# Optimization experiments

Hardware: AMD Instinct MI355X
Metric: run time of the kernel (lower is better)

## Reference

```python
import jax, jax.numpy as jnp
import numpy as np

WIN = 9
PAD = WIN // 2    # floor(9/2) = 4
WIN_SIZE = WIN * WIN
EPS = 1e-05


def _box_sum(x):
    # 9x9 ones-kernel conv, stride 1, pad 4 (SAME size), NCHW with C=1
    filt = jnp.ones((1, 1, WIN, WIN), dtype=x.dtype)
    return jax.lax.conv_general_dilated(
        x, filt, window_strides=(1, 1),
        padding=[(PAD, PAD), (PAD, PAD)],
        dimension_numbers=('NCHW', 'OIHW', 'NCHW'))


def setup_inputs() -> dict:
    key = jax.random.key(0)
    k1, k2 = jax.random.split(key)
    I = jax.random.normal(k1, (8, 1, 1024, 1024), dtype=jnp.float32)
    J = jax.random.normal(k2, (8, 1, 1024, 1024), dtype=jnp.float32)
    return {"I": I, "J": J}


def reference(I, J):
    I_sum = _box_sum(I)
    J_sum = _box_sum(J)
    I2_sum = _box_sum(I * I)
    J2_sum = _box_sum(J * J)
    IJ_sum = _box_sum(I * J)

    u_I = I_sum / WIN_SIZE
    u_J = J_sum / WIN_SIZE

    cross = IJ_sum - u_J * I_sum - u_I * J_sum + u_I * u_J * WIN_SIZE
    I_var = I2_sum - 2 * u_I * I_sum + u_I * u_I * WIN_SIZE
    J_var = J2_sum - 2 * u_J * J_sum + u_J * u_J * WIN_SIZE

    cc = cross * cross / (I_var * J_var + EPS)
    return jnp.mean(cc)
```

## Files before the change

### kernel.cpp

```cpp
#include <hip/hip_runtime.h>

#define H 1024
#define W 1024
#define NIMG 8
#define TX 128
#define CY 8
#define RS_ROWS (CY + 8)
#define NBX (W / TX)
#define NBY (H / CY)
#define NBLOCKS (NBX * NBY * NIMG)
#define EPS 1e-5f

__global__ __launch_bounds__(256, 4)
void ncc_main(const float* __restrict__ I, const float* __restrict__ J,
              float* __restrict__ partial) {
  __shared__ float4 rs4[RS_ROWS][TX];
  __shared__ float  rs1[RS_ROWS][TX];

  const int tid = threadIdx.x;
  const int gx = blockIdx.x, gy = blockIdx.y, n = blockIdx.z;
  const size_t img_off = (size_t)n * H * W;

  {
    const int r  = tid >> 4;
    const int xg = tid & 15;
    const int y  = gy * CY + r - 4;
    float a[16], b[16];
    if (y >= 0 && y < H) {
      const int xbase = gx * TX + xg * 8 - 4;
      const float* Ip = I + img_off + (size_t)y * W;
      const float* Jp = J + img_off + (size_t)y * W;
      if (xbase >= 0 && xbase + 16 <= W) {
        const float4* pa = reinterpret_cast<const float4*>(Ip + xbase);
        const float4* pb = reinterpret_cast<const float4*>(Jp + xbase);
        #pragma unroll
        for (int q = 0; q < 4; ++q) {
          float4 va = pa[q], vb = pb[q];
          a[4*q+0] = va.x; a[4*q+1] = va.y; a[4*q+2] = va.z; a[4*q+3] = va.w;
          b[4*q+0] = vb.x; b[4*q+1] = vb.y; b[4*q+2] = vb.z; b[4*q+3] = vb.w;
        }
      } else {
        #pragma unroll
        for (int k = 0; k < 16; ++k) {
          int xx = xbase + k;
          bool in = (xx >= 0) && (xx < W);
          a[k] = in ? Ip[xx] : 0.0f;
          b[k] = in ? Jp[xx] : 0.0f;
        }
      }
    } else {
      #pragma unroll
      for (int k = 0; k < 16; ++k) { a[k] = 0.0f; b[k] = 0.0f; }
    }
    float sI = 0.f, sJ = 0.f, sII = 0.f, sJJ = 0.f, sIJ = 0.f;
    #pragma unroll
    for (int k = 0; k < 9; ++k) {
      sI  += a[k];        sJ  += b[k];
      sII += a[k] * a[k]; sJJ += b[k] * b[k];
      sIJ += a[k] * b[k];
    }
    const int xg8 = xg * 8;
    const int xm  = xg & 7;
    #pragma unroll
    for (int i = 0; i < 8; ++i) {
      if (i > 0) {
        float an = a[i+8], al = a[i-1], bn = b[i+8], bl = b[i-1];
        sI  += an - al;           sJ  += bn - bl;
        sII += an*an - al*al;     sJJ += bn*bn - bl*bl;
        sIJ += an*bn - al*bl;
      }
      const int px = xg8 + (i ^ xm);
      rs4[r][px] = make_float4(sI, sJ, sII, sJJ);
      rs1[r][px] = sIJ;
    }
  }
  __syncthreads();

  const int x  = tid & 127;
  const int h  = tid >> 7;
  const int xs = (x & ~7) | ((x ^ (x >> 3)) & 7);
  const int base = h * 4;
  float4 rows4[9]; float rows1[9];
  float wI = 0.f, wJ = 0.f, wII = 0.f, wJJ = 0.f, wIJ = 0.f;
  #pragma unroll
  for (int k = 0; k < 9; ++k) {
    rows4[k] = rs4[base + k][xs];
    rows1[k] = rs1[base + k][xs];
    wI += rows4[k].x; wJ += rows4[k].y; wII += rows4[k].z; wJJ += rows4[k].w;
    wIJ += rows1[k];
  }
  const float inv81 = 1.0f / 81.0f;
  float acc = 0.f;
  #pragma unroll
  for (int i = 0; i < 4; ++i) {
    if (i > 0) {
      float4 e4 = rs4[base + 8 + i][xs];
      float  e1 = rs1[base + 8 + i][xs];
      wI  += e4.x - rows4[i-1].x;  wJ  += e4.y - rows4[i-1].y;
      wII += e4.z - rows4[i-1].z;  wJJ += e4.w - rows4[i-1].w;
      wIJ += e1   - rows1[i-1];
    }
    float cross = wIJ - wI * wJ * inv81;
    float Iv    = wII - wI * wI * inv81;
    float Jv    = wJJ - wJ * wJ * inv81;
    acc += cross * cross / (Iv * Jv + EPS);
  }

  #pragma unroll
  for (int off = 32; off > 0; off >>= 1)
    acc += __shfl_down(acc, off, 64);
  __syncthreads();
  if ((tid & 63) == 0) rs1[0][tid >> 6] = acc;
  __syncthreads();
  if (tid == 0) {
    const int blin = blockIdx.x + NBX * (blockIdx.y + NBY * (int)blockIdx.z);
    partial[blin] = rs1[0][0] + rs1[0][1] + rs1[0][2] + rs1[0][3];
  }
}

__global__ __launch_bounds__(256)
void ncc_reduce(const float* __restrict__ partial, float* __restrict__ out) {
  __shared__ float red[4];
  const int tid = threadIdx.x;
  float s = 0.f;
  #pragma unroll 8
  for (int i = tid; i < NBLOCKS; i += 256) s += partial[i];
  #pragma unroll
  for (int off = 32; off > 0; off >>= 1)
    s += __shfl_down(s, off, 64);
  if ((tid & 63) == 0) red[tid >> 6] = s;
  __syncthreads();
  if (tid == 0)
    out[0] = (red[0] + red[1] + red[2] + red[3]) *
             (1.0f / (float)((size_t)NIMG * H * W));
}

extern "C" void kernel_launch(void* const* d_in, const int* in_sizes, int n_in,
                              void* d_out, int out_size, void* d_ws, size_t ws_size,
                              hipStream_t stream) {
  const float* I = (const float*)d_in[0];
  const float* J = (const float*)d_in[1];
  float* out     = (float*)d_out;
  float* partial = (float*)d_ws;

  dim3 grid(NBX, NBY, NIMG);
  hipLaunchKernelGGL(ncc_main, grid, dim3(256), 0, stream, I, J, partial);
  hipLaunchKernelGGL(ncc_reduce, dim3(1), dim3(256), 0, stream, partial, out);
}
```

Baseline: 112.9 us.

## Stream tall row strips through a shared-memory ring with producer/consumer warps

Each block now covers a 64-row strip instead of 8 rows. Half the threads compute horizontal 9-wide sums for 8 new rows per iteration into a 16-slot shared ring buffer. The other half slide a vertical window down the strip and accumulate the NCC terms. This removes most of the redundant halo row loads and horizontal-sum work from the old 8-row tiles. The cost is fewer blocks, a serial loop with a barrier per iteration, and half the threads idle in each phase. The division is also replaced by a hardware reciprocal approximation, and the reduce unroll is lowered.

```diff
diff --git a/kernel.cpp b/kernel.cpp
--- a/kernel.cpp
+++ b/kernel.cpp
@@ -4,112 +4,143 @@
 #define W 1024
 #define NIMG 8
 #define TX 128
-#define CY 8
-#define RS_ROWS (CY + 8)
+#define STRIP 64
+#define NITER (STRIP / 8)
 #define NBX (W / TX)
-#define NBY (H / CY)
+#define NBY (H / STRIP)
 #define NBLOCKS (NBX * NBY * NIMG)
 #define EPS 1e-5f
+
+__device__ __forceinline__ void produce8(
+    const float* __restrict__ Ib, const float* __restrict__ Jb,
+    int y, int gx, int xg, int slot,
+    float4 (*rs4)[TX], float (*rs1)[TX])
+{
+  float a[16], b[16];
+  if (y >= 0 && y < H) {
+    const int xbase = gx * TX + xg * 8 - 4;
+    const float* Ip = Ib + (size_t)y * W;
+    const float* Jp = Jb + (size_t)y * W;
+    if (xbase >= 0 && xbase + 16 <= W) {
+      const float4* pa = reinterpret_cast<const float4*>(Ip + xbase);
+      const float4* pb = reinterpret_cast<const float4*>(Jp + xbase);
+      #pragma unroll
+      for (int q = 0; q < 4; ++q) {
+        float4 va = pa[q], vb = pb[q];
+        a[4*q+0] = va.x; a[4*q+1] = va.y; a[4*q+2] = va.z; a[4*q+3] = va.w;
+        b[4*q+0] = vb.x; b[4*q+1] = vb.y; b[4*q+2] = vb.z; b[4*q+3] = vb.w;
+      }
+    } else {
+      #pragma unroll
+      for (int k = 0; k < 16; ++k) {
+        int xx = xbase + k;
+        bool in = (xx >= 0) && (xx < W);
+        a[k] = in ? Ip[xx] : 0.0f;
+        b[k] = in ? Jp[xx] : 0.0f;
+      }
+    }
+  } else {
+    #pragma unroll
+    for (int k = 0; k < 16; ++k) { a[k] = 0.0f; b[k] = 0.0f; }
+  }
+  float sI = 0.f, sJ = 0.f, sII = 0.f, sJJ = 0.f, sIJ = 0.f;
+  #pragma unroll
+  for (int k = 0; k < 9; ++k) {
+    sI  += a[k];        sJ  += b[k];
+    sII += a[k] * a[k]; sJJ += b[k] * b[k];
+    sIJ += a[k] * b[k];
+  }
+  const int xg8 = xg * 8;
+  const int xm  = xg & 7;
+  #pragma unroll
+  for (int i = 0; i < 8; ++i) {
+    if (i > 0) {
+      float an = a[i+8], al = a[i-1], bn = b[i+8], bl = b[i-1];
+      sI  += an - al;           sJ  += bn - bl;
+      sII += an*an - al*al;     sJJ += bn*bn - bl*bl;
+      sIJ += an*bn - al*bl;
+    }
+    const int px = xg8 + (i ^ xm);
+    rs4[slot][px] = make_float4(sI, sJ, sII, sJJ);
+    rs1[slot][px] = sIJ;
+  }
+}
 
 __global__ __launch_bounds__(256, 4)
 void ncc_main(const float* __restrict__ I, const float* __restrict__ J,
               float* __restrict__ partial) {
-  __shared__ float4 rs4[RS_ROWS][TX];
-  __shared__ float  rs1[RS_ROWS][TX];
+  __shared__ float4 rs4[16][TX];
+  __shared__ float  rs1[16][TX];
 
   const int tid = threadIdx.x;
-  const int gx = blockIdx.x, gy = blockIdx.y, n = blockIdx.z;
+  const int gx = blockIdx.x, sy = blockIdx.y, n = blockIdx.z;
+  const int y0 = sy * STRIP;
   const size_t img_off = (size_t)n * H * W;
+  const float* Ib = I + img_off;
+  const float* Jb = J + img_off;
 
   {
-    const int r  = tid >> 4;
+    const int rr = tid >> 4;
     const int xg = tid & 15;
-    const int y  = gy * CY + r - 4;
-    float a[16], b[16];
-    if (y >= 0 && y < H) {
-      const int xbase = gx * TX + xg * 8 - 4;
-      const float* Ip = I + img_off + (size_t)y * W;
-      const float* Jp = J + img_off + (size_t)y * W;
-      if (xbase >= 0 && xbase + 16 <= W) {
-        const float4* pa = reinterpret_cast<const float4*>(Ip + xbase);
-        const float4* pb = reinterpret_cast<const float4*>(Jp + xbase);
-        #pragma unroll
-        for (int q = 0; q < 4; ++q) {
-          float4 va = pa[q], vb = pb[q];
-          a[4*q+0] = va.x; a[4*q+1] = va.y; a[4*q+2] = va.z; a[4*q+3] = va.w;
-          b[4*q+0] = vb.x; b[4*q+1] = vb.y; b[4*q+2] = vb.z; b[4*q+3] = vb.w;
-        }
-      } else {
-        #pragma unroll
-        for (int k = 0; k < 16; ++k) {
-          int xx = xbase + k;
-          bool in = (xx >= 0) && (xx < W);
-          a[k] = in ? Ip[xx] : 0.0f;
-          b[k] = in ? Jp[xx] : 0.0f;
-        }
-      }
-    } else {
-      #pragma unroll
-      for (int k = 0; k < 16; ++k) { a[k] = 0.0f; b[k] = 0.0f; }
-    }
-    float sI = 0.f, sJ = 0.f, sII = 0.f, sJJ = 0.f, sIJ = 0.f;
+    produce8(Ib, Jb, y0 - 4 + rr, gx, xg, (rr + 12) & 15, rs4, rs1);
+  }
+  __syncthreads();
+
+  const int col = tid - 128;
+  const int xs  = (col & ~7) | ((col ^ (col >> 3)) & 7);
+  float4 h4[9]; float h1[9];
+  float wI = 0.f, wJ = 0.f, wII = 0.f, wJJ = 0.f, wIJ = 0.f;
+  float acc = 0.f;
+  if (tid >= 128) {
+    h4[0] = make_float4(0.f, 0.f, 0.f, 0.f); h1[0] = 0.f;
     #pragma unroll
-    for (int k = 0; k < 9; ++k) {
-      sI  += a[k];        sJ  += b[k];
-      sII += a[k] * a[k]; sJJ += b[k] * b[k];
-      sIJ += a[k] * b[k];
-    }
-    const int xg8 = xg * 8;
-    const int xm  = xg & 7;
-    #pragma unroll
-    for (int i = 0; i < 8; ++i) {
-      if (i > 0) {
-        float an = a[i+8], al = a[i-1], bn = b[i+8], bl = b[i-1];
-        sI  += an - al;           sJ  += bn - bl;
-        sII += an*an - al*al;     sJJ += bn*bn - bl*bl;
-        sIJ += an*bn - al*bl;
-      }
-      const int px = xg8 + (i ^ xm);
-      rs4[r][px] = make_float4(sI, sJ, sII, sJJ);
-      rs1[r][px] = sIJ;
+    for (int j = 0; j < 8; ++j) {
+      const int s = (j + 12) & 15;
+      h4[j+1] = rs4[s][xs]; h1[j+1] = rs1[s][xs];
+      wI += h4[j+1].x; wJ += h4[j+1].y; wII += h4[j+1].z; wJJ += h4[j+1].w;
+      wIJ += h1[j+1];
     }
   }
   __syncthreads();
 
-  const int x  = tid & 127;
-  const int h  = tid >> 7;
-  const int xs = (x & ~7) | ((x ^ (x >> 3)) & 7);
-  const int base = h * 4;
-  float4 rows4[9]; float rows1[9];
-  float wI = 0.f, wJ = 0.f, wII = 0.f, wJJ = 0.f, wIJ = 0.f;
-  #pragma unroll
-  for (int k = 0; k < 9; ++k) {
-    rows4[k] = rs4[base + k][xs];
-    rows1[k] = rs1[base + k][xs];
-    wI += rows4[k].x; wJ += rows4[k].y; wII += rows4[k].z; wJJ += rows4[k].w;
-    wIJ += rows1[k];
-  }
   const float inv81 = 1.0f / 81.0f;
-  float acc = 0.f;
-  #pragma unroll
-  for (int i = 0; i < 4; ++i) {
-    if (i > 0) {
-      float4 e4 = rs4[base + 8 + i][xs];
-      float  e1 = rs1[base + 8 + i][xs];
-      wI  += e4.x - rows4[i-1].x;  wJ  += e4.y - rows4[i-1].y;
-      wII += e4.z - rows4[i-1].z;  wJJ += e4.w - rows4[i-1].w;
-      wIJ += e1   - rows1[i-1];
+  for (int t = 0; t < NITER; ++t) {
+    if (tid < 128) {
+      if (t < NITER - 1) {
+        const int r  = tid >> 4;
+        const int xg = tid & 15;
+        const int rel = 8*t + 12 + r;
+        produce8(Ib, Jb, y0 + rel, gx, xg, rel & 15, rs4, rs1);
+      }
+    } else {
+      const int sb = (8*t + 4) & 15;
+      float4 n4[8]; float n1[8];
+      #pragma unroll
+      for (int j = 0; j < 8; ++j) {
+        const int s = (sb + j) & 15;
+        n4[j] = rs4[s][xs]; n1[j] = rs1[s][xs];
+      }
+      #pragma unroll
+      for (int i = 0; i < 8; ++i) {
+        wI  += n4[i].x - h4[i].x;  wJ  += n4[i].y - h4[i].y;
+        wII += n4[i].z - h4[i].z;  wJJ += n4[i].w - h4[i].w;
+        wIJ += n1[i]   - h1[i];
+        float cross = fmaf(-(wI * wJ), inv81, wIJ);
+        float Iv    = fmaf(-(wI * wI), inv81, wII);
+        float Jv    = fmaf(-(wJ * wJ), inv81, wJJ);
+        acc = fmaf(cross * cross,
+                   __builtin_amdgcn_rcpf(fmaf(Iv, Jv, EPS)), acc);
+      }
+      h4[0] = h4[8]; h1[0] = h1[8];
+      #pragma unroll
+      for (int j = 1; j < 9; ++j) { h4[j] = n4[j-1]; h1[j] = n1[j-1]; }
     }
-    float cross = wIJ - wI * wJ * inv81;
-    float Iv    = wII - wI * wI * inv81;
-    float Jv    = wJJ - wJ * wJ * inv81;
-    acc += cross * cross / (Iv * Jv + EPS);
+    __syncthreads();
   }
 
   #pragma unroll
   for (int off = 32; off > 0; off >>= 1)
     acc += __shfl_down(acc, off, 64);
-  __syncthreads();
   if ((tid & 63) == 0) rs1[0][tid >> 6] = acc;
   __syncthreads();
   if (tid == 0) {
@@ -123,7 +154,7 @@
   __shared__ float red[4];
   const int tid = threadIdx.x;
   float s = 0.f;
-  #pragma unroll 8
+  #pragma unroll 4
   for (int i = tid; i < NBLOCKS; i += 256) s += partial[i];
   #pragma unroll
   for (int off = 32; off > 0; off >>= 1)
```

New measurement: 125.1 us. 10.8% more time.
